# Kernel optimization log

Measured on AMD Instinct MI355X. Metric: run time of the kernel, lower is better.

## Reference

```python
import jax, jax.numpy as jnp
import numpy as np

N, E, F_IN, E_IN, H, L, C = 50000, 500000, 128, 16, 128, 2, 2
BN_EPS = 1e-5


def _linear_params(key, fan_in, fan_out):
    k1, k2 = jax.random.split(key)
    w = jax.random.normal(k1, (fan_in, fan_out), jnp.float32) * (1.0 / np.sqrt(fan_in))
    b = jax.random.normal(k2, (fan_out,), jnp.float32) * 0.01
    return w, b


def setup_inputs() -> dict:
    key = jax.random.key(0)
    ks = jax.random.split(key, 32)
    x = jax.random.normal(ks[0], (N, F_IN), jnp.float32)
    edge_attr = jax.random.normal(ks[1], (E, E_IN), jnp.float32)
    edge_index = jax.random.randint(ks[2], (2, E), 0, N, jnp.int64)

    node_w, node_b = _linear_params(ks[3], F_IN, H)
    edge_w, edge_b = _linear_params(ks[4], E_IN, H)

    def stack(fn, base):
        ws, bs = zip(*[fn(jax.random.fold_in(ks[base], i)) for i in range(L)])
        return jnp.stack(ws), jnp.stack(bs)

    conv_w1, conv_b1 = stack(lambda k: _linear_params(k, H, H), 5)
    conv_w2, conv_b2 = stack(lambda k: _linear_params(k, H, H), 6)
    emlp_w1, emlp_b1 = stack(lambda k: _linear_params(k, 3 * H, H), 7)
    emlp_w2, emlp_b2 = stack(lambda k: _linear_params(k, H, H), 8)
    bn_gamma = jnp.ones((L, H), jnp.float32)
    bn_beta = jnp.zeros((L, H), jnp.float32)

    mlp_w1, mlp_b1 = _linear_params(ks[9], 3 * H, 50)
    mlp_w2, mlp_b2 = _linear_params(ks[10], 50, 25)
    mlp_w3, mlp_b3 = _linear_params(ks[11], 25, C)

    return dict(x=x, edge_attr=edge_attr,
                node_w=node_w, node_b=node_b, edge_w=edge_w, edge_b=edge_b,
                conv_w1=conv_w1, conv_b1=conv_b1, conv_w2=conv_w2, conv_b2=conv_b2,
                bn_gamma=bn_gamma, bn_beta=bn_beta,
                emlp_w1=emlp_w1, emlp_b1=emlp_b1, emlp_w2=emlp_w2, emlp_b2=emlp_b2,
                mlp_w1=mlp_w1, mlp_b1=mlp_b1, mlp_w2=mlp_w2, mlp_b2=mlp_b2,
                mlp_w3=mlp_w3, mlp_b3=mlp_b3, edge_index=edge_index)


def _forward(x, edge_attr, node_w, node_b, edge_w, edge_b,
             conv_w1, conv_b1, conv_w2, conv_b2, bn_gamma, bn_beta,
             emlp_w1, emlp_b1, emlp_w2, emlp_b2,
             mlp_w1, mlp_b1, mlp_w2, mlp_b2, mlp_w3, mlp_b3, edge_index):
    src, dst = edge_index[0], edge_index[1]
    h = x @ node_w + node_b                      # [N, H]
    ea = edge_attr @ edge_w + edge_b             # [E, H]
    for i in range(L):
        # GINEConv: message = relu(x_src + edge_attr), scatter-add at dst
        msg = jax.nn.relu(h[src] + ea)           # [E, H]
        agg = jax.ops.segment_sum(msg, dst, num_segments=N)
        z = h + agg                              # eps = 0
        z = jax.nn.relu(z @ conv_w1[i] + conv_b1[i]) @ conv_w2[i] + conv_b2[i]
        # BatchNorm (training-mode batch statistics over nodes)
        mu = jnp.mean(z, axis=0)
        var = jnp.var(z, axis=0)
        z = bn_gamma[i] * (z - mu) * jax.lax.rsqrt(var + BN_EPS) + bn_beta[i]
        h = (h + jax.nn.relu(z)) * 0.5
        # edge update MLP
        eu = jnp.concatenate([h[src], h[dst], ea], axis=-1)  # [E, 3H]
        ea = ea + (jax.nn.relu(eu @ emlp_w1[i] + emlp_b1[i]) @ emlp_w2[i] + emlp_b2[i]) * 0.5
    # readout: x[edge_index.T].reshape(-1, 2H) cat edge_attr -> [E, 3H]
    feat = jnp.concatenate([h[src], h[dst], ea], axis=-1)
    o = jax.nn.relu(feat @ mlp_w1 + mlp_b1)      # dropout is eval no-op
    o = jax.nn.relu(o @ mlp_w2 + mlp_b2)
    return o @ mlp_w3 + mlp_b3                   # [E, n_classes]


def reference(x, edge_attr, node_w, node_b, edge_w, edge_b,
              conv_w1, conv_b1, conv_w2, conv_b2, bn_gamma, bn_beta,
              emlp_w1, emlp_b1, emlp_w2, emlp_b2,
              mlp_w1, mlp_b1, mlp_w2, mlp_b2, mlp_w3, mlp_b3, edge_index):
    return _forward(x, edge_attr, node_w, node_b, edge_w, edge_b,
                    conv_w1, conv_b1, conv_w2, conv_b2, bn_gamma, bn_beta,
                    emlp_w1, emlp_b1, emlp_w2, emlp_b2,
                    mlp_w1, mlp_b1, mlp_w2, mlp_b2, mlp_w3, mlp_b3, edge_index)
```

## Files before the change

kernel.cpp:

```cpp
#include <hip/hip_runtime.h>


#define NN 50000
#define NE 500000
#define HD 128

typedef _Float16 f16;
typedef _Float16 f16x8 __attribute__((ext_vector_type(8)));
typedef _Float16 f16x4 __attribute__((ext_vector_type(4)));
typedef _Float16 f16x2 __attribute__((ext_vector_type(2)));
typedef float f32x4 __attribute__((ext_vector_type(4)));
typedef unsigned short ushort_t;

#define MFMA16(a, b, c) __builtin_amdgcn_mfma_f32_16x16x32_f16((a), (b), (c), 0, 0, 0)

#define TSTR 152

#define P_NODE_W 0
#define P_NODE_B 16384
#define P_EDGE_W 16512
#define P_EDGE_B 18560
#define P_CONV_W1 18688
#define P_CONV_B1 51456
#define P_CONV_W2 51712
#define P_CONV_B2 84480
#define P_GAMMA 84736
#define P_BETA 84992
#define P_EMLP_W1 85248
#define P_EMLP_B1 183552
#define P_EMLP_W2 183808
#define P_EMLP_B2 216576
#define P_MLP_W1 216832
#define P_MLP_B1 236032
#define P_MLP_W2 236082
#define P_MLP_B2 237332
#define P_MLP_W3 237357
#define P_MLP_B3 237407
#define P_TOTAL 237409

__device__ __forceinline__ float bf2f(unsigned short u) {
    union { unsigned int i; float f; } v;
    v.i = ((unsigned int)u) << 16;
    return v.f;
}

__global__ __launch_bounds__(256) void k_detect(
    const unsigned int* nw, const int* ei, int* flags) {
    __shared__ int cF, cI;
    if (threadIdx.x == 0) { cF = 0; cI = 0; }
    __syncthreads();
    unsigned int u = nw[threadIdx.x];
    int e = (int)((u >> 7) & 0xFFu);
    int odd = ei[2 * threadIdx.x + 1];
    if (e >= 100 && e <= 140) atomicAdd(&cF, 1);
    if (odd != 0) atomicAdd(&cI, 1);
    __syncthreads();
    if (threadIdx.x == 0) {
        flags[0] = (cF < 160) ? 1 : 0;
        flags[1] = (cI < 64) ? 1 : 0;
    }
}

__global__ __launch_bounds__(256) void k_cvt(
    const void* src, f16* dst, int n4, const int* flags) {
    int i = blockIdx.x * 256 + threadIdx.x;
    if (i >= n4) return;
    f16x4 o;
    if (flags[0]) {
        float4 v = ((const float4*)src)[i];
        o[0] = (f16)v.x; o[1] = (f16)v.y; o[2] = (f16)v.z; o[3] = (f16)v.w;
    } else {
        ushort4 v = ((const ushort4*)src)[i];
        o[0] = (f16)bf2f(v.x); o[1] = (f16)bf2f(v.y);
        o[2] = (f16)bf2f(v.z); o[3] = (f16)bf2f(v.w);
    }
    ((f16x4*)dst)[i] = o;
}

__global__ __launch_bounds__(256) void k_cvt_prm(
    const void* p0, const void* p1, const void* p2, const void* p3,
    const void* p4, const void* p5, const void* p6, const void* p7,
    const void* p8, const void* p9, const void* p10, const void* p11,
    const void* p12, const void* p13, const void* p14, const void* p15,
    const void* p16, const void* p17, const void* p18, const void* p19,
    float* prm, const int* flags) {
    int i = blockIdx.x * 256 + threadIdx.x;
    if (i >= P_TOTAL) return;
    const int offs[21] = {P_NODE_W, P_NODE_B, P_EDGE_W, P_EDGE_B, P_CONV_W1,
                          P_CONV_B1, P_CONV_W2, P_CONV_B2, P_GAMMA, P_BETA,
                          P_EMLP_W1, P_EMLP_B1, P_EMLP_W2, P_EMLP_B2, P_MLP_W1,
                          P_MLP_B1, P_MLP_W2, P_MLP_B2, P_MLP_W3, P_MLP_B3,
                          P_TOTAL};
    const void* srcs[20] = {p0, p1, p2, p3, p4, p5, p6, p7, p8, p9, p10, p11,
                            p12, p13, p14, p15, p16, p17, p18, p19};
    int s = 0;
#pragma unroll
    for (int k = 1; k < 20; ++k)
        if (i >= offs[k]) s = k;
    int li = i - offs[s];
    float v = flags[0] ? ((const float*)srcs[s])[li]
                       : bf2f(((const ushort_t*)srcs[s])[li]);
    prm[i] = v;
}

__global__ __launch_bounds__(256) void k_cvt_idx(
    const int* src, int* dst, const int* flags) {
    int i = blockIdx.x * 256 + threadIdx.x;
    if (i >= 2 * NE) return;
    dst[i] = flags[1] ? src[2 * i] : src[i];
}

__global__ __launch_bounds__(256) void k_hist(const int* eix, int* cnt) {
    int e = blockIdx.x * 256 + threadIdx.x;
    if (e < NE) atomicAdd(&cnt[eix[NE + e]], 1);
}

__global__ __launch_bounds__(256) void k_scanA(const int* cnt, int* bsum) {
    __shared__ int wsum[4];
    int tid = threadIdx.x;
    int i = blockIdx.x * 256 + tid;
    int v = (i < NN) ? cnt[i] : 0;
#pragma unroll
    for (int s = 1; s < 64; s <<= 1) v += __shfl_xor(v, s);
    if ((tid & 63) == 0) wsum[tid >> 6] = v;
    __syncthreads();
    if (tid == 0) bsum[blockIdx.x] = wsum[0] + wsum[1] + wsum[2] + wsum[3];
}

__global__ __launch_bounds__(256) void k_scanB(const int* bsum, int* bpre, int* off) {
    __shared__ int l[200];
    int tid = threadIdx.x;
    if (tid < 196) l[tid] = bsum[tid];
    __syncthreads();
    if (tid == 0) {
        int run = 0;
        for (int b = 0; b < 196; ++b) { int t = l[b]; l[b] = run; run += t; }
        off[NN] = run;
    }
    __syncthreads();
    if (tid < 196) bpre[tid] = l[tid];
}

__global__ __launch_bounds__(256) void k_scanC(
    const int* cnt, const int* bpre, int* off, int* cursor) {
    __shared__ int wsum[4];
    int tid = threadIdx.x;
    int lane = tid & 63, wave = tid >> 6;
    int i = blockIdx.x * 256 + tid;
    int v = (i < NN) ? cnt[i] : 0;
    int incl = v;
#pragma unroll
    for (int s = 1; s < 64; s <<= 1) {
        int t = __shfl_up(incl, s);
        if (lane >= s) incl += t;
    }
    if (lane == 63) wsum[wave] = incl;
    __syncthreads();
    int add = bpre[blockIdx.x];
    for (int w = 0; w < 4; ++w)
        if (w < wave) add += wsum[w];
    int excl = add + incl - v;
    if (i < NN) { off[i] = excl; cursor[i] = excl; }
}

__global__ __launch_bounds__(256) void k_scatter(
    const int* eix, int* cursor, int* eord) {
    int e = blockIdx.x * 256 + threadIdx.x;
    if (e >= NE) return;
    int d = eix[NE + e];
    int pos = atomicAdd(&cursor[d], 1);
    eord[pos] = e;
}

__global__ __launch_bounds__(256) void k_agg(
    const f16* ea, const f16* h16, const int* eix, const int* off,
    const int* eord, f16* agg16) {
    int wid = (blockIdx.x * 256 + threadIdx.x) >> 6;
    int lane = threadIdx.x & 63;
    int beg = off[wid], end = off[wid + 1];
    float a0 = 0.f, a1 = 0.f;
    for (int i = beg; i < end; ++i) {
        int e = eord[i];
        int s = eix[e];
        f16x2 ev = *(const f16x2*)(ea + (size_t)e * HD + lane * 2);
        f16x2 hv = *(const f16x2*)(h16 + (size_t)s * HD + lane * 2);
        a0 += fmaxf((float)ev[0] + (float)hv[0], 0.f);
        a1 += fmaxf((float)ev[1] + (float)hv[1], 0.f);
    }
    f16x2 o; o[0] = (f16)a0; o[1] = (f16)a1;
    *(f16x2*)(agg16 + (size_t)wid * HD + lane * 2) = o;
}

__global__ __launch_bounds__(256) void k_prep(const float* prm, f16* wbuf) {
    int gid = blockIdx.x * 256 + threadIdx.x;
    if (gid < 13 * 16384) {
        int seg = gid >> 14;
        int idx = gid & 16383;
        int off;
        switch (seg) {
            case 0: off = P_NODE_W; break;
            case 1: off = P_CONV_W1; break;
            case 2: off = P_CONV_W1 + 16384; break;
            case 3: off = P_CONV_W2; break;
            case 4: off = P_CONV_W2 + 16384; break;
            case 5: case 6: case 7: off = P_EMLP_W1 + (seg - 5) * 16384; break;
            case 8: case 9: case 10: off = P_EMLP_W1 + 49152 + (seg - 8) * 16384; break;
            case 11: off = P_EMLP_W2; break;
            default: off = P_EMLP_W2 + 16384; break;
        }
        int fb = idx >> 9;
        int sub = (idx & 511) >> 3;
        int j = idx & 7;
        int q = sub >> 4, n = sub & 15;
        int nt = fb >> 2, kt = fb & 3;
        int k = kt * 32 + q * 8 + j;
        int c = nt * 16 + n;
        wbuf[gid] = (f16)prm[off + k * 128 + c];
    } else {
        int t = gid - 13 * 16384;
        if (t >= 3 * 8192) return;
        int s = t >> 13;
        int idx = t & 8191;
        int fb = idx >> 9;
        int sub = (idx & 511) >> 3;
        int j = idx & 7;
        int q = sub >> 4, n = sub & 15;
        int nt = fb >> 2, kt = fb & 3;
        int k = s * 128 + kt * 32 + q * 8 + j;
        int c = nt * 16 + n;
        float v = (c < 50) ? prm[P_MLP_W1 + k * 50 + c] : 0.f;
        wbuf[13 * 16384 + s * 8192 + idx] = (f16)v;
    }
}

__global__ __launch_bounds__(256) void k_node_lin(
    const f16* xc, const f16* wT, const float* bias, f16* h_f16) {
    __shared__ __align__(16) f16 wlds[16384];
    int tid = threadIdx.x;
    {
        const uint4* s = (const uint4*)wT;
        uint4* d = (uint4*)wlds;
        for (int i = tid; i < 2048; i += 256) d[i] = s[i];
    }
    __syncthreads();
    int wave = tid >> 6, lane = tid & 63, q = lane >> 4, ln = lane & 15;
    int rowbase = blockIdx.x * 128 + wave * 32;
    f32x4 acc[2][8] = {};
#pragma unroll
    for (int kt = 0; kt < 4; ++kt) {
        int koff = kt * 32 + q * 8;
        f16x8 a[2];
#pragma unroll
        for (int mt = 0; mt < 2; ++mt) {
            int row = min(rowbase + mt * 16 + ln, NN - 1);
            a[mt] = *(const f16x8*)(xc + row * HD + koff);
        }
#pragma unroll
        for (int nt = 0; nt < 8; ++nt) {
            f16x8 b = *(const f16x8*)&wlds[(nt * 4 + kt) * 512 + lane * 8];
            acc[0][nt] = MFMA16(a[0], b, acc[0][nt]);
            acc[1][nt] = MFMA16(a[1], b, acc[1][nt]);
        }
    }
#pragma unroll
    for (int nt = 0; nt < 8; ++nt) {
        int col = nt * 16 + ln;
        float bv = bias[col];
#pragma unroll
        for (int mt = 0; mt < 2; ++mt)
#pragma unroll
            for (int r = 0; r < 4; ++r) {
                int row = rowbase + mt * 16 + q * 4 + r;
                if (row < NN) h_f16[row * HD + col] = (f16)(acc[mt][nt][r] + bv);
            }
    }
}

__global__ __launch_bounds__(256) void k_edge_lin(
    const f16* eattr, const float* ew, const float* ebias, f16* ea) {
    __shared__ float wl[16 * 128];
    __shared__ float bl[128];
    __shared__ float al[64 * 16];
    int tid = threadIdx.x;
    int eb = blockIdx.x * 64;
    for (int i = tid; i < 2048; i += 256) wl[i] = ew[i];
    if (tid < 128) bl[tid] = ebias[tid];
    {
        int e_l = tid >> 2, k0 = (tid & 3) * 4;
        int e = min(eb + e_l, NE - 1);
        f16x4 u = *(const f16x4*)(eattr + e * 16 + k0);
        al[e_l * 16 + k0 + 0] = (float)u[0];
        al[e_l * 16 + k0 + 1] = (float)u[1];
        al[e_l * 16 + k0 + 2] = (float)u[2];
        al[e_l * 16 + k0 + 3] = (float)u[3];
    }
    __syncthreads();
    for (int i = 0; i < 32; ++i) {
        int o = i * 256 + tid;
        int e_l = o >> 7, c = o & 127;
        float s = bl[c];
#pragma unroll
        for (int k = 0; k < 16; ++k) s += al[e_l * 16 + k] * wl[k * 128 + c];
        int e = eb + e_l;
        if (e < NE) ea[(size_t)e * HD + c] = (f16)s;
    }
}

__global__ __launch_bounds__(256) void k_conv1(
    const f16* h16, const f16* agg16, const f16* wT, const float* bias,
    f16* t_node) {
    __shared__ __align__(16) f16 wlds[16384];
    int tid = threadIdx.x;
    {
        const uint4* s = (const uint4*)wT;
        uint4* d = (uint4*)wlds;
        for (int i = tid; i < 2048; i += 256) d[i] = s[i];
    }
    __syncthreads();
    int wave = tid >> 6, lane = tid & 63, q = lane >> 4, ln = lane & 15;
    int rowbase = blockIdx.x * 128 + wave * 32;
    f32x4 acc[2][8] = {};
#pragma unroll
    for (int kt = 0; kt < 4; ++kt) {
        int koff = kt * 32 + q * 8;
        f16x8 a[2];
#pragma unroll
        for (int mt = 0; mt < 2; ++mt) {
            int row = min(rowbase + mt * 16 + ln, NN - 1);
            f16x8 hv = *(const f16x8*)(h16 + row * HD + koff);
            f16x8 gv = *(const f16x8*)(agg16 + row * HD + koff);
            f16x8 av;
#pragma unroll
            for (int j = 0; j < 8; ++j) av[j] = (f16)((float)hv[j] + (float)gv[j]);
            a[mt] = av;
        }
#pragma unroll
        for (int nt = 0; nt < 8; ++nt) {
            f16x8 b = *(const f16x8*)&wlds[(nt * 4 + kt) * 512 + lane * 8];
            acc[0][nt] = MFMA16(a[0], b, acc[0][nt]);
            acc[1][nt] = MFMA16(a[1], b, acc[1][nt]);
        }
    }
#pragma unroll
    for (int nt = 0; nt < 8; ++nt) {
        int col = nt * 16 + ln;
        float bv = bias[col];
#pragma unroll
        for (int mt = 0; mt < 2; ++mt)
#pragma unroll
            for (int r = 0; r < 4; ++r) {
                int row = rowbase + mt * 16 + q * 4 + r;
                if (row < NN)
                    t_node[row * HD + col] = (f16)fmaxf(acc[mt][nt][r] + bv, 0.f);
            }
    }
}

__global__ __launch_bounds__(256) void k_conv2(
    const f16* t_node, const f16* wT, const float* bias, f16* z2, float* stats) {
    __shared__ __align__(16) f16 wlds[16384];
    int tid = threadIdx.x;
    {
        const uint4* s = (const uint4*)wT;
        uint4* d = (uint4*)wlds;
        for (int i = tid; i < 2048; i += 256) d[i] = s[i];
    }
    __syncthreads();
    int wave = tid >> 6, lane = tid & 63, q = lane >> 4, ln = lane & 15;
    int rowbase = blockIdx.x * 128 + wave * 32;
    f32x4 acc[2][8] = {};
#pragma unroll
    for (int kt = 0; kt < 4; ++kt) {
        int koff = kt * 32 + q * 8;
        f16x8 a[2];
#pragma unroll
        for (int mt = 0; mt < 2; ++mt) {
            int row = min(rowbase + mt * 16 + ln, NN - 1);
            a[mt] = *(const f16x8*)(t_node + row * HD + koff);
        }
#pragma unroll
        for (int nt = 0; nt < 8; ++nt) {
            f16x8 b = *(const f16x8*)&wlds[(nt * 4 + kt) * 512 + lane * 8];
            acc[0][nt] = MFMA16(a[0], b, acc[0][nt]);
            acc[1][nt] = MFMA16(a[1], b, acc[1][nt]);
        }
    }
#pragma unroll
    for (int nt = 0; nt < 8; ++nt) {
        int col = nt * 16 + ln;
        float bv = bias[col];
        float s = 0.f, s2 = 0.f;
#pragma unroll
        for (int mt = 0; mt < 2; ++mt)
#pragma unroll
            for (int r = 0; r < 4; ++r) {
                int row = rowbase + mt * 16 + q * 4 + r;
                if (row < NN) {
                    float v = acc[mt][nt][r] + bv;
                    z2[row * HD + col] = (f16)v;
                    s += v;
                    s2 += v * v;
                }
            }
        s += __shfl_xor(s, 16);  s += __shfl_xor(s, 32);
        s2 += __shfl_xor(s2, 16); s2 += __shfl_xor(s2, 32);
        if (lane < 16) {
            atomicAdd(&stats[col], s);
            atomicAdd(&stats[HD + col], s2);
        }
    }
}

__global__ __launch_bounds__(256) void k_bn(
    const f16* z2, const float* stats, const float* gamma, const float* beta,
    f16* h16) {
    int gid = blockIdx.x * 256 + threadIdx.x;
    if (gid >= NN * HD / 4) return;
    int base = gid * 4;
    int c0 = base & (HD - 1);
    f16x4 z = *(const f16x4*)(z2 + base);
    f16x4 h = *(const f16x4*)(h16 + base);
    f16x4 ho;
#pragma unroll
    for (int j = 0; j < 4; ++j) {
        int c = c0 + j;
        float mu = stats[c] * (1.0f / NN);
        float var = stats[HD + c] * (1.0f / NN) - mu * mu;
        float zn = gamma[c] * ((float)z[j] - mu) * rsqrtf(var + 1e-5f) + beta[c];
        ho[j] = (f16)(((float)h[j] + fmaxf(zn, 0.f)) * 0.5f);
    }
    *(f16x4*)(h16 + base) = ho;
}

__global__ __launch_bounds__(256, 4) void k_emlp(
    const f16* h16, const int* eidx, const f16* w1T, const float* b1,
    const f16* w2T, const float* b2, f16* ea) {
    __shared__ __align__(16) f16 wlds[16384];
    __shared__ int sidx[128], didx[128];
    int tid = threadIdx.x;
    int eb = blockIdx.x * 128;
    if (tid < 128) {
        int e = min(eb + tid, NE - 1);
        sidx[tid] = eidx[e];
        didx[tid] = eidx[NE + e];
    }
    int wave = tid >> 6, lane = tid & 63, q = lane >> 4, ln = lane & 15;
    int el0 = wave * 32 + ln;
    int el1 = wave * 32 + 16 + ln;
    f32x4 acc[2][8] = {};
    for (int seg = 0; seg < 3; ++seg) {
        __syncthreads();
        {
            const uint4* s = (const uint4*)(w1T + seg * 16384);
            uint4* d = (uint4*)wlds;
            for (int i = tid; i < 2048; i += 256) d[i] = s[i];
        }
        __syncthreads();
        const f16 *p0, *p1;
        if (seg == 0) {
            p0 = h16 + (size_t)sidx[el0] * HD;
            p1 = h16 + (size_t)sidx[el1] * HD;
        } else if (seg == 1) {
            p0 = h16 + (size_t)didx[el0] * HD;
            p1 = h16 + (size_t)didx[el1] * HD;
        } else {
            p0 = ea + (size_t)min(eb + el0, NE - 1) * HD;
            p1 = ea + (size_t)min(eb + el1, NE - 1) * HD;
        }
        f16x8 g0[4], g1[4];
#pragma unroll
        for (int kt = 0; kt < 4; ++kt) {
            g0[kt] = *(const f16x8*)(p0 + kt * 32 + q * 8);
            g1[kt] = *(const f16x8*)(p1 + kt * 32 + q * 8);
        }
#pragma unroll
        for (int kt = 0; kt < 4; ++kt)
#pragma unroll
            for (int mt = 0; mt < 8; ++mt) {
                f16x8 a = *(const f16x8*)&wlds[(mt * 4 + kt) * 512 + lane * 8];
                acc[0][mt] = MFMA16(a, g0[kt], acc[0][mt]);
                acc[1][mt] = MFMA16(a, g1[kt], acc[1][mt]);
            }
    }
    union HU { f16 h; unsigned short u; };
    unsigned int pk[2][4][4];
#pragma unroll
    for (int ntl = 0; ntl < 2; ++ntl)
#pragma unroll
        for (int kt = 0; kt < 4; ++kt) {
            f32x4 blo = *(const f32x4*)(b1 + (2 * kt) * 16 + q * 4);
            f32x4 bhi = *(const f32x4*)(b1 + (2 * kt + 1) * 16 + q * 4);
#pragma unroll
            for (int r = 0; r < 4; ++r) {
                HU lo, hi;
                lo.h = (f16)fmaxf(acc[ntl][2 * kt][r] + blo[r], 0.f);
                hi.h = (f16)fmaxf(acc[ntl][2 * kt + 1][r] + bhi[r], 0.f);
                pk[ntl][kt][r] =
                    (unsigned int)lo.u | ((unsigned int)hi.u << 16);
            }
        }
    __syncthreads();
    {
        const uint4* s = (const uint4*)w2T;
        uint4* d = (uint4*)wlds;
        for (int i = tid; i < 2048; i += 256) d[i] = s[i];
    }
    __syncthreads();
    int s1 = (((2 * q) & 3) << 4) | ln;
    int s2 = (((2 * q + 1) & 3) << 4) | ln;
    int hsh = (q >> 1) * 16;
    f32x4 acc2[2][8] = {};
#pragma unroll
    for (int kt = 0; kt < 4; ++kt) {
        f16x8 bf[2];
#pragma unroll
        for (int ntl = 0; ntl < 2; ++ntl) {
            union { unsigned short u[8]; f16x8 v; } bb;
#pragma unroll
            for (int r = 0; r < 4; ++r) {
                unsigned int v1 = (unsigned int)__shfl((int)pk[ntl][kt][r], s1);
                unsigned int v2 = (unsigned int)__shfl((int)pk[ntl][kt][r], s2);
                bb.u[r] = (unsigned short)(v1 >> hsh);
                bb.u[4 + r] = (unsigned short)(v2 >> hsh);
            }
            bf[ntl] = bb.v;
        }
#pragma unroll
        for (int mt = 0; mt < 8; ++mt) {
            f16x8 a = *(const f16x8*)&wlds[(mt * 4 + kt) * 512 + lane * 8];
            acc2[0][mt] = MFMA16(a, bf[0], acc2[0][mt]);
            acc2[1][mt] = MFMA16(a, bf[1], acc2[1][mt]);
        }
    }
#pragma unroll
    for (int ntl = 0; ntl < 2; ++ntl) {
        int e = eb + wave * 32 + ntl * 16 + ln;
        if (e < NE) {
            f16* erow = ea + (size_t)e * HD;
#pragma unroll
            for (int mt = 0; mt < 8; ++mt) {
                int c0 = mt * 16 + q * 4;
                f32x4 bv = *(const f32x4*)(b2 + c0);
                f16x4 old = *(const f16x4*)(erow + c0);
                f16x4 nw;
#pragma unroll
                for (int r = 0; r < 4; ++r)
                    nw[r] = (f16)((float)old[r] +
                                  0.5f * (acc2[ntl][mt][r] + bv[r]));
                *(f16x4*)(erow + c0) = nw;
            }
        }
    }
}

__global__ __launch_bounds__(256) void k_readout(
    const f16* h16, const f16* ea, const int* eidx, const f16* w1Tp,
    const float* mb1, const float* mw2, const float* mb2,
    const float* mw3, const float* mb3, float* out) {
    __shared__ __align__(16) f16 wlds[8192];
    __shared__ f16 o1[256 * 58];
    __shared__ float w2l[50 * 28];
    __shared__ float w3l[50];
    __shared__ float b2l[25];
    __shared__ float b3l[2];
    __shared__ int sidx[256], didx[256];
    int tid = threadIdx.x;
    int eb = blockIdx.x * 256;
    {
        int e = min(eb + tid, NE - 1);
        sidx[tid] = eidx[e];
        didx[tid] = eidx[NE + e];
    }
    for (int i = tid; i < 50 * 28; i += 256) {
        int k = i / 28, ko = i - k * 28;
        w2l[i] = (ko < 25) ? mw2[k * 25 + ko] : 0.f;
    }
    if (tid < 50) w3l[tid] = mw3[tid];
    if (tid < 25) b2l[tid] = mb2[tid];
    if (tid < 2) b3l[tid] = mb3[tid];
    int wave = tid >> 6, lane = tid & 63, q = lane >> 4, ln = lane & 15;
    f32x4 acc[4][4] = {};
    for (int seg = 0; seg < 3; ++seg) {
        __syncthreads();
        {
            const uint4* s = (const uint4*)(w1Tp + seg * 8192);
            uint4* d = (uint4*)wlds;
            for (int i = tid; i < 1024; i += 256) d[i] = s[i];
        }
        __syncthreads();
#pragma unroll
        for (int kt = 0; kt < 4; ++kt) {
            int koff = kt * 32 + q * 8;
            f16x8 a[4];
#pragma unroll
            for (int mt = 0; mt < 4; ++mt) {
                int le = wave * 64 + mt * 16 + ln;
                const f16* ap;
                if (seg == 0)      ap = h16 + (size_t)sidx[le] * HD + koff;
                else if (seg == 1) ap = h16 + (size_t)didx[le] * HD + koff;
                else               ap = ea + (size_t)min(eb + le, NE - 1) * HD + koff;
                a[mt] = *(const f16x8*)ap;
            }
#pragma unroll
            for (int nt = 0; nt < 4; ++nt) {
                f16x8 b = *(const f16x8*)&wlds[(nt * 4 + kt) * 512 + lane * 8];
#pragma unroll
                for (int mt = 0; mt < 4; ++mt)
                    acc[mt][nt] = MFMA16(a[mt], b, acc[mt][nt]);
            }
        }
    }
#pragma unroll
    for (int nt = 0; nt < 4; ++nt) {
        int col = nt * 16 + ln;
        if (col < 50) {
            float bv = mb1[col];
#pragma unroll
            for (int mt = 0; mt < 4; ++mt)
#pragma unroll
                for (int r = 0; r < 4; ++r) {
                    int le = wave * 64 + mt * 16 + q * 4 + r;
                    o1[le * 58 + col] = (f16)fmaxf(acc[mt][nt][r] + bv, 0.f);
                }
        }
    }
    __syncthreads();
    float o2[25];
#pragma unroll
    for (int ko = 0; ko < 25; ++ko) o2[ko] = b2l[ko];
    for (int k = 0; k < 50; ++k) {
        float a = (float)o1[tid * 58 + k];
#pragma unroll
        for (int ko = 0; ko < 25; ++ko) o2[ko] += a * w2l[k * 28 + ko];
    }
    float r0 = b3l[0], r1 = b3l[1];
#pragma unroll
    for (int ko = 0; ko < 25; ++ko) {
        float a = fmaxf(o2[ko], 0.f);
        r0 += a * w3l[ko * 2];
        r1 += a * w3l[ko * 2 + 1];
    }
    int e = eb + tid;
    if (e < NE) {
        float2 o; o.x = r0; o.y = r1;
        *(float2*)(out + (size_t)e * 2) = o;
    }
}

extern "C" void kernel_launch(void* const* d_in, const int* in_sizes, int n_in,
                              void* d_out, int out_size, void* d_ws, size_t ws_size,
                              hipStream_t stream) {
    const size_t WS_NEED = 197425936ULL;
    if (ws_size < WS_NEED) {
        hipMemsetAsync(d_out, 0, (size_t)out_size * 4, stream);
        return;
    }
    char* ws = (char*)d_ws;
    f16* ea = (f16*)(ws);
    f16* hf16 = (f16*)(ws + 128000000LL);
    f16* agg16 = (f16*)(ws + 140800000LL);
    f16* eattr16 = (f16*)(ws + 140800000LL);
    int* eord = (int*)(ws + 153600000LL);
    int* off = (int*)(ws + 155600000LL);
    int* cntcur = (int*)(ws + 155800064LL);
    int* bsum = (int*)(ws + 156000064LL);
    int* bpre = (int*)(ws + 156001088LL);
    f16* z2 = (f16*)(ws + 166400000LL);
    f16* xc = (f16*)(ws + 166400000LL);
    f16* tn = (f16*)(ws + 179200000LL);
    f16* wbuf = (f16*)(ws + 192000000LL);
    float* stats = (float*)(ws + 192475136LL);
    float* prm = (float*)(ws + 192476160LL);
    int* eix = (int*)(ws + 193425920LL);
    int* flags = (int*)(ws + 197425920LL);
    float* out = (float*)d_out;

    k_detect<<<1, 256, 0, stream>>>((const unsigned int*)d_in[2],
                                    (const int*)d_in[22], flags);
    k_cvt<<<6250, 256, 0, stream>>>(d_in[0], xc, 1600000, flags);
    k_cvt<<<7813, 256, 0, stream>>>(d_in[1], eattr16, 2000000, flags);
    k_cvt_prm<<<928, 256, 0, stream>>>(
        d_in[2], d_in[3], d_in[4], d_in[5], d_in[6], d_in[7], d_in[8], d_in[9],
        d_in[10], d_in[11], d_in[12], d_in[13], d_in[14], d_in[15], d_in[16],
        d_in[17], d_in[18], d_in[19], d_in[20], d_in[21], prm, flags);
    k_cvt_idx<<<3907, 256, 0, stream>>>((const int*)d_in[22], eix, flags);

    k_prep<<<928, 256, 0, stream>>>(prm, wbuf);
    k_node_lin<<<391, 256, 0, stream>>>(xc, wbuf, prm + P_NODE_B, hf16);
    k_edge_lin<<<7813, 256, 0, stream>>>(eattr16, prm + P_EDGE_W, prm + P_EDGE_B, ea);

    hipMemsetAsync(cntcur, 0, NN * 4, stream);
    k_hist<<<1954, 256, 0, stream>>>(eix, cntcur);
    k_scanA<<<196, 256, 0, stream>>>(cntcur, bsum);
    k_scanB<<<1, 256, 0, stream>>>(bsum, bpre, off);
    k_scanC<<<196, 256, 0, stream>>>(cntcur, bpre, off, cntcur);
    k_scatter<<<1954, 256, 0, stream>>>(eix, cntcur, eord);

    for (int l = 0; l < 2; ++l) {
        hipMemsetAsync(stats, 0, 1024, stream);
        k_agg<<<12500, 256, 0, stream>>>(ea, hf16, eix, off, eord, agg16);
        k_conv1<<<391, 256, 0, stream>>>(hf16, agg16, wbuf + (1 + l) * 16384,
                                         prm + P_CONV_B1 + l * HD, tn);
        k_conv2<<<391, 256, 0, stream>>>(tn, wbuf + (3 + l) * 16384,
                                         prm + P_CONV_B2 + l * HD, z2, stats);
        k_bn<<<6250, 256, 0, stream>>>(z2, stats, prm + P_GAMMA + l * HD,
                                       prm + P_BETA + l * HD, hf16);
        k_emlp<<<3907, 256, 0, stream>>>(hf16, eix, wbuf + (5 + l * 3) * 16384,
                                         prm + P_EMLP_B1 + l * HD,
                                         wbuf + (11 + l) * 16384,
                                         prm + P_EMLP_B2 + l * HD, ea);
    }
    k_readout<<<1954, 256, 0, stream>>>(hf16, ea, eix, wbuf + 13 * 16384,
                                        prm + P_MLP_B1, prm + P_MLP_W2,
                                        prm + P_MLP_B2, prm + P_MLP_W3,
                                        prm + P_MLP_B3, out);
}
```

Measured before the change: 1.021 ms.

## Store edge features in destination-sorted order to make aggregation reads contiguous

Edges are permuted into CSR (destination-sorted) order once, so the edge feature buffer, source and destination index arrays are all kept in sorted order. Aggregation then streams edge features contiguously instead of gathering them through the permutation, and the edge MLP and readout read indices from the presorted arrays. The readout scatters outputs back through the permutation. This trades a gather in the edge linear step and a scattered output write for contiguous reads in the per-layer aggregation, and it moves buffer placements in the workspace.

```diff
diff --git a/kernel.cpp b/kernel.cpp
--- a/kernel.cpp
+++ b/kernel.cpp
@@ -13,8 +13,6 @@
 typedef unsigned short ushort_t;
 
 #define MFMA16(a, b, c) __builtin_amdgcn_mfma_f32_16x16x32_f16((a), (b), (c), 0, 0, 0)
-
-#define TSTR 152
 
 #define P_NODE_W 0
 #define P_NODE_B 16384
@@ -172,17 +170,24 @@
     eord[pos] = e;
 }
 
+__global__ __launch_bounds__(256) void k_gidx(
+    const int* eix, const int* eord, int* ssrc, int* sdst) {
+    int i = blockIdx.x * 256 + threadIdx.x;
+    if (i >= NE) return;
+    int e = eord[i];
+    ssrc[i] = eix[e];
+    sdst[i] = eix[NE + e];
+}
+
 __global__ __launch_bounds__(256) void k_agg(
-    const f16* ea, const f16* h16, const int* eix, const int* off,
-    const int* eord, f16* agg16) {
+    const f16* ea, const f16* h16, const int* ssrc, const int* off, f16* agg16) {
     int wid = (blockIdx.x * 256 + threadIdx.x) >> 6;
     int lane = threadIdx.x & 63;
     int beg = off[wid], end = off[wid + 1];
     float a0 = 0.f, a1 = 0.f;
     for (int i = beg; i < end; ++i) {
-        int e = eord[i];
-        int s = eix[e];
-        f16x2 ev = *(const f16x2*)(ea + (size_t)e * HD + lane * 2);
+        int s = ssrc[i];
+        f16x2 ev = *(const f16x2*)(ea + (size_t)i * HD + lane * 2);
         f16x2 hv = *(const f16x2*)(h16 + (size_t)s * HD + lane * 2);
         a0 += fmaxf((float)ev[0] + (float)hv[0], 0.f);
         a1 += fmaxf((float)ev[1] + (float)hv[1], 0.f);
@@ -277,7 +282,8 @@
 }
 
 __global__ __launch_bounds__(256) void k_edge_lin(
-    const f16* eattr, const float* ew, const float* ebias, f16* ea) {
+    const f16* eattr, const float* ew, const float* ebias, const int* eord,
+    f16* ea) {
     __shared__ float wl[16 * 128];
     __shared__ float bl[128];
     __shared__ float al[64 * 16];
@@ -287,8 +293,8 @@
     if (tid < 128) bl[tid] = ebias[tid];
     {
         int e_l = tid >> 2, k0 = (tid & 3) * 4;
-        int e = min(eb + e_l, NE - 1);
-        f16x4 u = *(const f16x4*)(eattr + e * 16 + k0);
+        int er = eord[min(eb + e_l, NE - 1)];
+        f16x4 u = *(const f16x4*)(eattr + er * 16 + k0);
         al[e_l * 16 + k0 + 0] = (float)u[0];
         al[e_l * 16 + k0 + 1] = (float)u[1];
         al[e_l * 16 + k0 + 2] = (float)u[2];
@@ -433,20 +439,16 @@
 }
 
 __global__ __launch_bounds__(256, 4) void k_emlp(
-    const f16* h16, const int* eidx, const f16* w1T, const float* b1,
-    const f16* w2T, const float* b2, f16* ea) {
+    const f16* h16, const int* ssrc, const int* sdst, const f16* w1T,
+    const float* b1, const f16* w2T, const float* b2, f16* ea) {
     __shared__ __align__(16) f16 wlds[16384];
-    __shared__ int sidx[128], didx[128];
     int tid = threadIdx.x;
     int eb = blockIdx.x * 128;
-    if (tid < 128) {
-        int e = min(eb + tid, NE - 1);
-        sidx[tid] = eidx[e];
-        didx[tid] = eidx[NE + e];
-    }
     int wave = tid >> 6, lane = tid & 63, q = lane >> 4, ln = lane & 15;
-    int el0 = wave * 32 + ln;
-    int el1 = wave * 32 + 16 + ln;
+    int g0 = min(eb + wave * 32 + ln, NE - 1);
+    int g1 = min(eb + wave * 32 + 16 + ln, NE - 1);
+    int is0 = ssrc[g0], is1 = ssrc[g1];
+    int id0 = sdst[g0], id1 = sdst[g1];
     f32x4 acc[2][8] = {};
     for (int seg = 0; seg < 3; ++seg) {
         __syncthreads();
@@ -458,28 +460,28 @@
         __syncthreads();
         const f16 *p0, *p1;
         if (seg == 0) {
-            p0 = h16 + (size_t)sidx[el0] * HD;
-            p1 = h16 + (size_t)sidx[el1] * HD;
+            p0 = h16 + (size_t)is0 * HD;
+            p1 = h16 + (size_t)is1 * HD;
         } else if (seg == 1) {
-            p0 = h16 + (size_t)didx[el0] * HD;
-            p1 = h16 + (size_t)didx[el1] * HD;
+            p0 = h16 + (size_t)id0 * HD;
+            p1 = h16 + (size_t)id1 * HD;
         } else {
-            p0 = ea + (size_t)min(eb + el0, NE - 1) * HD;
-            p1 = ea + (size_t)min(eb + el1, NE - 1) * HD;
-        }
-        f16x8 g0[4], g1[4];
+            p0 = ea + (size_t)g0 * HD;
+            p1 = ea + (size_t)g1 * HD;
+        }
+        f16x8 f0[4], f1[4];
 #pragma unroll
         for (int kt = 0; kt < 4; ++kt) {
-            g0[kt] = *(const f16x8*)(p0 + kt * 32 + q * 8);
-            g1[kt] = *(const f16x8*)(p1 + kt * 32 + q * 8);
+            f0[kt] = *(const f16x8*)(p0 + kt * 32 + q * 8);
+            f1[kt] = *(const f16x8*)(p1 + kt * 32 + q * 8);
         }
 #pragma unroll
         for (int kt = 0; kt < 4; ++kt)
 #pragma unroll
             for (int mt = 0; mt < 8; ++mt) {
                 f16x8 a = *(const f16x8*)&wlds[(mt * 4 + kt) * 512 + lane * 8];
-                acc[0][mt] = MFMA16(a, g0[kt], acc[0][mt]);
-                acc[1][mt] = MFMA16(a, g1[kt], acc[1][mt]);
+                acc[0][mt] = MFMA16(a, f0[kt], acc[0][mt]);
+                acc[1][mt] = MFMA16(a, f1[kt], acc[1][mt]);
             }
     }
     union HU { f16 h; unsigned short u; };
@@ -554,9 +556,9 @@
 }
 
 __global__ __launch_bounds__(256) void k_readout(
-    const f16* h16, const f16* ea, const int* eidx, const f16* w1Tp,
-    const float* mb1, const float* mw2, const float* mb2,
-    const float* mw3, const float* mb3, float* out) {
+    const f16* h16, const f16* ea, const int* ssrc, const int* sdst,
+    const int* eord, const f16* w1Tp, const float* mb1, const float* mw2,
+    const float* mb2, const float* mw3, const float* mb3, float* out) {
     __shared__ __align__(16) f16 wlds[8192];
     __shared__ f16 o1[256 * 58];
     __shared__ float w2l[50 * 28];
@@ -568,8 +570,8 @@
     int eb = blockIdx.x * 256;
     {
         int e = min(eb + tid, NE - 1);
-        sidx[tid] = eidx[e];
-        didx[tid] = eidx[NE + e];
+        sidx[tid] = ssrc[e];
+        didx[tid] = sdst[e];
     }
     for (int i = tid; i < 50 * 28; i += 256) {
         int k = i / 28, ko = i - k * 28;
@@ -642,8 +644,9 @@
     }
     int e = eb + tid;
     if (e < NE) {
+        int oe = eord[e];
         float2 o; o.x = r0; o.y = r1;
-        *(float2*)(out + (size_t)e * 2) = o;
+        *(float2*)(out + (size_t)oe * 2) = o;
     }
 }
 
@@ -659,14 +662,16 @@
     f16* ea = (f16*)(ws);
     f16* hf16 = (f16*)(ws + 128000000LL);
     f16* agg16 = (f16*)(ws + 140800000LL);
-    f16* eattr16 = (f16*)(ws + 140800000LL);
+    f16* xc = (f16*)(ws + 140800000LL);
     int* eord = (int*)(ws + 153600000LL);
     int* off = (int*)(ws + 155600000LL);
     int* cntcur = (int*)(ws + 155800064LL);
     int* bsum = (int*)(ws + 156000064LL);
     int* bpre = (int*)(ws + 156001088LL);
+    int* ssrc = (int*)(ws + 156002176LL);
+    int* sdst = (int*)(ws + 158002176LL);
+    f16* eattr16 = (f16*)(ws + 166400000LL);
     f16* z2 = (f16*)(ws + 166400000LL);
-    f16* xc = (f16*)(ws + 166400000LL);
     f16* tn = (f16*)(ws + 179200000LL);
     f16* wbuf = (f16*)(ws + 192000000LL);
     float* stats = (float*)(ws + 192475136LL);
@@ -685,32 +690,36 @@
         d_in[17], d_in[18], d_in[19], d_in[20], d_in[21], prm, flags);
     k_cvt_idx<<<3907, 256, 0, stream>>>((const int*)d_in[22], eix, flags);
 
-    k_prep<<<928, 256, 0, stream>>>(prm, wbuf);
-    k_node_lin<<<391, 256, 0, stream>>>(xc, wbuf, prm + P_NODE_B, hf16);
-    k_edge_lin<<<7813, 256, 0, stream>>>(eattr16, prm + P_EDGE_W, prm + P_EDGE_B, ea);
-
     hipMemsetAsync(cntcur, 0, NN * 4, stream);
     k_hist<<<1954, 256, 0, stream>>>(eix, cntcur);
     k_scanA<<<196, 256, 0, stream>>>(cntcur, bsum);
     k_scanB<<<1, 256, 0, stream>>>(bsum, bpre, off);
     k_scanC<<<196, 256, 0, stream>>>(cntcur, bpre, off, cntcur);
     k_scatter<<<1954, 256, 0, stream>>>(eix, cntcur, eord);
+    k_gidx<<<1954, 256, 0, stream>>>(eix, eord, ssrc, sdst);
+
+    k_prep<<<928, 256, 0, stream>>>(prm, wbuf);
+    k_node_lin<<<391, 256, 0, stream>>>(xc, wbuf, prm + P_NODE_B, hf16);
+    k_edge_lin<<<7813, 256, 0, stream>>>(eattr16, prm + P_EDGE_W, prm + P_EDGE_B,
+                                         eord, ea);
 
     for (int l = 0; l < 2; ++l) {
         hipMemsetAsync(stats, 0, 1024, stream);
-        k_agg<<<12500, 256, 0, stream>>>(ea, hf16, eix, off, eord, agg16);
+        k_agg<<<12500, 256, 0, stream>>>(ea, hf16, ssrc, off, agg16);
         k_conv1<<<391, 256, 0, stream>>>(hf16, agg16, wbuf + (1 + l) * 16384,
                                          prm + P_CONV_B1 + l * HD, tn);
         k_conv2<<<391, 256, 0, stream>>>(tn, wbuf + (3 + l) * 16384,
                                          prm + P_CONV_B2 + l * HD, z2, stats);
         k_bn<<<6250, 256, 0, stream>>>(z2, stats, prm + P_GAMMA + l * HD,
                                        prm + P_BETA + l * HD, hf16);
-        k_emlp<<<3907, 256, 0, stream>>>(hf16, eix, wbuf + (5 + l * 3) * 16384,
+        k_emlp<<<3907, 256, 0, stream>>>(hf16, ssrc, sdst,
+                                         wbuf + (5 + l * 3) * 16384,
                                          prm + P_EMLP_B1 + l * HD,
                                          wbuf + (11 + l) * 16384,
                                          prm + P_EMLP_B2 + l * HD, ea);
     }
-    k_readout<<<1954, 256, 0, stream>>>(hf16, ea, eix, wbuf + 13 * 16384,
+    k_readout<<<1954, 256, 0, stream>>>(hf16, ea, ssrc, sdst, eord,
+                                        wbuf + 13 * 16384,
                                         prm + P_MLP_B1, prm + P_MLP_W2,
                                         prm + P_MLP_B2, prm + P_MLP_W3,
                                         prm + P_MLP_B3, out);
```

Result: faster. 966.4 us (-5.3%).
